# Performance work log

Hardware: AMD Instinct MI355X
Metric: run time of the kernel (lower is better)

The kernel has to match this reference:

```python
import jax, jax.numpy as jnp
import numpy as np

R = 1.1
SCALE = 100.0
BUMP_STEPS = 32
NUM_THETAS = 32
NUM_FEATURES = 128
N_NODES = 200000
NUM_GRAPHS = 128


def setup_inputs() -> dict:
    key = jax.random.key(0)
    k1, k2, k3 = jax.random.split(key, 3)
    x = jax.random.normal(k1, (N_NODES, NUM_FEATURES), dtype=jnp.float32)
    batch = jnp.sort(jax.random.randint(k2, (N_NODES,), 0, NUM_GRAPHS, dtype=jnp.int64))
    v = jax.random.uniform(k3, (NUM_THETAS, NUM_FEATURES), dtype=jnp.float32) - 0.5
    return {"x": x, "batch": batch, "num_graphs": NUM_GRAPHS, "v": v}


def reference(x, batch, num_graphs, v):
    # nh: node heights along each direction theta -> [N, T]
    nh = x @ v.T
    # linspace over filtration values -> [S]
    lin = jnp.linspace(-R, R, BUMP_STEPS, dtype=nh.dtype)
    # bump: sigmoid difference; second point is the constant pad value R
    # ecc: [N, S, T]  (node-major so segment_sum reduces the leading axis)
    ecc = (jax.nn.sigmoid(SCALE * (lin[None, :, None] - nh[:, None, :]))
           - jax.nn.sigmoid(SCALE * (lin - R))[None, :, None])
    # scatter-add per graph label -> [ng, S, T] == index_add over dim1 then movedim(0,1)
    ect = jax.ops.segment_sum(ecc, batch, num_segments=num_graphs)
    return ect
```

## Files before the change

kernel.cpp:

```cpp
#include <hip/hip_runtime.h>
#include <math.h>

#define N_NODES 200000
#define NF 128
#define NT 32
#define NS 32
#define NG 128
#define SPLITS 32
#define ATILE 64
#define ABLOCKS 3125
#define KSTRIDE 136
#define HPAD 33

typedef short bf16x8 __attribute__((ext_vector_type(8)));
typedef float floatx4 __attribute__((ext_vector_type(4)));

__device__ __forceinline__ float rcp_fast(float x) { return __builtin_amdgcn_rcpf(x); }

__device__ __forceinline__ void split_bf16(float f, unsigned short& h, unsigned short& l) {
    unsigned u  = __float_as_uint(f);
    unsigned r  = u + 0x7FFFu + ((u >> 16) & 1u);
    unsigned hb = r & 0xFFFF0000u;
    h = (unsigned short)(hb >> 16);
    float rem = f - __uint_as_float(hb);
    unsigned u2 = __float_as_uint(rem);
    unsigned r2 = u2 + 0x7FFFu + ((u2 >> 16) & 1u);
    l = (unsigned short)(r2 >> 16);
}

__global__ __launch_bounds__(256)
void offsets_kernel(const int* __restrict__ batch, int* __restrict__ off)
{
    int i = blockIdx.x * 256 + threadIdx.x;
    if (i >= N_NODES) return;
    int b  = batch[i];
    int bp = (i == 0) ? -1 : batch[i - 1];
    for (int g = bp + 1; g <= b; ++g) off[g] = i;
    if (i == N_NODES - 1)
        for (int g = b + 1; g <= NG; ++g) off[g] = N_NODES;
}

__global__ __launch_bounds__(256, 2)
void gemm_kernel(const float* __restrict__ x,
                 const float* __restrict__ v,
                 float* __restrict__ nh)
{
    __shared__ unsigned short xh[ATILE * KSTRIDE];
    __shared__ unsigned short xl[ATILE * KSTRIDE];
    __shared__ unsigned short vh[NT * KSTRIDE];
    __shared__ unsigned short vl[NT * KSTRIDE];

    const int tid = threadIdx.x;
    const int blk = blockIdx.x;

    #pragma unroll
    for (int j = 0; j < 8; ++j) {
        int idx4 = j * 256 + tid;
        int nn   = idx4 >> 5;
        int f4   = idx4 & 31;
        float4 val = *(const float4*)&x[(size_t)(blk * ATILE + nn) * NF + f4 * 4];
        unsigned short h0,h1,h2,h3,l0,l1,l2,l3;
        split_bf16(val.x, h0, l0); split_bf16(val.y, h1, l1);
        split_bf16(val.z, h2, l2); split_bf16(val.w, h3, l3);
        uint2 hh, ll;
        hh.x = (unsigned)h0 | ((unsigned)h1 << 16); hh.y = (unsigned)h2 | ((unsigned)h3 << 16);
        ll.x = (unsigned)l0 | ((unsigned)l1 << 16); ll.y = (unsigned)l2 | ((unsigned)l3 << 16);
        *(uint2*)&xh[nn * KSTRIDE + f4 * 4] = hh;
        *(uint2*)&xl[nn * KSTRIDE + f4 * 4] = ll;
    }
    #pragma unroll
    for (int j = 0; j < 4; ++j) {
        int idx4 = j * 256 + tid;
        int row  = idx4 >> 5;
        int f4   = idx4 & 31;
        float4 val = *(const float4*)&v[(size_t)row * NF + f4 * 4];
        unsigned short h0,h1,h2,h3,l0,l1,l2,l3;
        split_bf16(val.x, h0, l0); split_bf16(val.y, h1, l1);
        split_bf16(val.z, h2, l2); split_bf16(val.w, h3, l3);
        uint2 hh, ll;
        hh.x = (unsigned)h0 | ((unsigned)h1 << 16); hh.y = (unsigned)h2 | ((unsigned)h3 << 16);
        ll.x = (unsigned)l0 | ((unsigned)l1 << 16); ll.y = (unsigned)l2 | ((unsigned)l3 << 16);
        *(uint2*)&vh[row * KSTRIDE + f4 * 4] = hh;
        *(uint2*)&vl[row * KSTRIDE + f4 * 4] = ll;
    }
    __syncthreads();

    const int w    = tid >> 6;
    const int lane = tid & 63;
    const int mrow = lane & 15;
    const int quad = lane >> 4;

    const int abase  = (w * 16 + mrow) * KSTRIDE + quad * 8;
    const int b0base = mrow * KSTRIDE + quad * 8;
    const int b1base = (16 + mrow) * KSTRIDE + quad * 8;

    floatx4 acc0 = {0.f, 0.f, 0.f, 0.f};
    floatx4 acc1 = {0.f, 0.f, 0.f, 0.f};

    #pragma unroll
    for (int slice = 0; slice < 4; ++slice) {
        bf16x8 ah  = *(bf16x8*)&xh[abase  + slice * 32];
        bf16x8 al  = *(bf16x8*)&xl[abase  + slice * 32];
        bf16x8 bh0 = *(bf16x8*)&vh[b0base + slice * 32];
        bf16x8 bl0 = *(bf16x8*)&vl[b0base + slice * 32];
        bf16x8 bh1 = *(bf16x8*)&vh[b1base + slice * 32];
        bf16x8 bl1 = *(bf16x8*)&vl[b1base + slice * 32];
        acc0 = __builtin_amdgcn_mfma_f32_16x16x32_bf16(ah, bh0, acc0, 0, 0, 0);
        acc0 = __builtin_amdgcn_mfma_f32_16x16x32_bf16(ah, bl0, acc0, 0, 0, 0);
        acc0 = __builtin_amdgcn_mfma_f32_16x16x32_bf16(al, bh0, acc0, 0, 0, 0);
        acc1 = __builtin_amdgcn_mfma_f32_16x16x32_bf16(ah, bh1, acc1, 0, 0, 0);
        acc1 = __builtin_amdgcn_mfma_f32_16x16x32_bf16(ah, bl1, acc1, 0, 0, 0);
        acc1 = __builtin_amdgcn_mfma_f32_16x16x32_bf16(al, bh1, acc1, 0, 0, 0);
    }

    #pragma unroll
    for (int reg = 0; reg < 4; ++reg) {
        size_t node = (size_t)blk * ATILE + w * 16 + quad * 4 + reg;
        nh[node * NT + mrow]      = acc0[reg];
        nh[node * NT + 16 + mrow] = acc1[reg];
    }
}

__global__ __launch_bounds__(256, 8)
void sweep_kernel(const float* __restrict__ nh,
                  const int* __restrict__ off,
                  float* __restrict__ out)
{
    __shared__ unsigned hist[NT * HPAD];
    __shared__ float    corr[NT * HPAD];

    const int tid   = threadIdx.x;
    const int g     = blockIdx.x >> 5;
    const int split = blockIdx.x & (SPLITS - 1);

    for (int i = tid; i < NT * HPAD; i += 256) { hist[i] = 0u; corr[i] = 0.0f; }
    __syncthreads();

    const int g_start = off[g];
    const int g_end   = off[g + 1];
    const int count   = g_end - g_start;
    const int chunk   = (count + SPLITS - 1) / SPLITS;
    int my_start = g_start + split * chunk;
    if (my_start > g_end) my_start = g_end;
    int my_end = my_start + chunk;
    if (my_end > g_end) my_end = g_end;
    const int my_count = my_end - my_start;

    const float inv_dlin = 14.090909090909092f;
    const float Lw       = 10.23848093f;
    const float dlin     = 2.2f / 31.0f;
    const float L        = 144.26950408889634f;

    const int t = tid & 31;
    const int r = tid >> 5;

    for (int j = my_start + r; j < my_end; j += 8) {
        float h = nh[(size_t)j * NT + t];
        float z = fmaf(h, inv_dlin, 15.5f);
        int s_up = (int)ceilf(z);
        s_up = min(max(s_up, 0), 32);
        atomicAdd(&hist[t * HPAD + s_up], 1u);
        int s0 = (int)ceilf(z - 1.45f);
        #pragma unroll
        for (int i2 = 0; i2 < 3; ++i2) {
            int s = s0 + i2;
            float e   = __builtin_amdgcn_exp2f(Lw * (z - (float)s));
            float sig = rcp_fast(1.0f + e);
            float stp = (s >= s_up) ? 1.0f : 0.0f;
            float c   = sig - stp;
            if (s >= 0 && s <= 31) atomicAdd(&corr[t * HPAD + s], c);
        }
    }
    __syncthreads();

    {
        const int grp = tid >> 5;
        const int s   = tid & 31;
        for (int row = grp; row < NT; row += 8) {
            float val = (float)hist[row * HPAD + s];
            #pragma unroll
            for (int d = 1; d < 32; d <<= 1) {
                float nbr = __shfl_up(val, d, 32);
                if (s >= d) val += nbr;
            }
            corr[row * HPAD + s] += val;
        }
    }
    __syncthreads();

    const int sb = tid >> 5;
    #pragma unroll
    for (int k = 0; k < 4; ++k) {
        int s = sb + 8 * k;
        float lin_s = -1.1f + (float)s * dlin;
        float cs  = rcp_fast(1.0f + __builtin_amdgcn_exp2f(L * (1.1f - lin_s)));
        float val = corr[t * HPAD + s] - (float)my_count * cs;
        atomicAdd(&out[(size_t)g * (NS * NT) + s * NT + t], val);
    }
}

extern "C" void kernel_launch(void* const* d_in, const int* in_sizes, int n_in,
                              void* d_out, int out_size, void* d_ws, size_t ws_size,
                              hipStream_t stream) {
    const float* x     = (const float*)d_in[0];
    const int*   batch = (const int*)d_in[1];
    const float* v     = (const float*)d_in[3];
    float*       out   = (float*)d_out;

    int*   offs = (int*)d_ws;
    float* nh   = (float*)((char*)d_ws + 1024);

    hipMemsetAsync(d_out, 0, (size_t)out_size * sizeof(float), stream);
    offsets_kernel<<<dim3((N_NODES + 255) / 256), dim3(256), 0, stream>>>(batch, offs);
    gemm_kernel<<<dim3(ABLOCKS), dim3(256), 0, stream>>>(x, v, nh);
    sweep_kernel<<<dim3(NG * SPLITS), dim3(256), 0, stream>>>(nh, offs, out);
}
```

Before: 198.5 us.

## Fuse offsets, GEMM and histogram sweep into a single per-tile kernel

Replaces the offsets, GEMM and sweep kernels with one kernel. Each 64-node tile computes node heights in MFMA accumulators and immediately builds per-graph histograms and corrections in LDS, then atomically adds them to the output. This removes the global round trip of the node-height array, the offsets pass and two launches, and loads x straight into registers instead of staging it in LDS. The cost is extra per-tile work: a histogram clear, prefix scan and 1024 global atomics for every graph a tile touches. Global atomic contention on the output stays roughly the same as before.

```diff
diff --git a/kernel.cpp b/kernel.cpp
--- a/kernel.cpp
+++ b/kernel.cpp
@@ -6,10 +6,9 @@
 #define NT 32
 #define NS 32
 #define NG 128
-#define SPLITS 32
 #define ATILE 64
 #define ABLOCKS 3125
-#define KSTRIDE 136
+#define VSTRIDE 136
 #define HPAD 33
 
 typedef short bf16x8 __attribute__((ext_vector_type(8)));
@@ -28,46 +27,38 @@
     l = (unsigned short)(r2 >> 16);
 }
 
-__global__ __launch_bounds__(256)
-void offsets_kernel(const int* __restrict__ batch, int* __restrict__ off)
-{
-    int i = blockIdx.x * 256 + threadIdx.x;
-    if (i >= N_NODES) return;
-    int b  = batch[i];
-    int bp = (i == 0) ? -1 : batch[i - 1];
-    for (int g = bp + 1; g <= b; ++g) off[g] = i;
-    if (i == N_NODES - 1)
-        for (int g = b + 1; g <= NG; ++g) off[g] = N_NODES;
+__device__ __forceinline__ void split8(float4 a, float4 b, bf16x8& h8, bf16x8& l8) {
+    unsigned short h[8], l[8];
+    split_bf16(a.x, h[0], l[0]); split_bf16(a.y, h[1], l[1]);
+    split_bf16(a.z, h[2], l[2]); split_bf16(a.w, h[3], l[3]);
+    split_bf16(b.x, h[4], l[4]); split_bf16(b.y, h[5], l[5]);
+    split_bf16(b.z, h[6], l[6]); split_bf16(b.w, h[7], l[7]);
+    h8 = (bf16x8){(short)h[0],(short)h[1],(short)h[2],(short)h[3],
+                  (short)h[4],(short)h[5],(short)h[6],(short)h[7]};
+    l8 = (bf16x8){(short)l[0],(short)l[1],(short)l[2],(short)l[3],
+                  (short)l[4],(short)l[5],(short)l[6],(short)l[7]};
 }
 
-__global__ __launch_bounds__(256, 2)
-void gemm_kernel(const float* __restrict__ x,
-                 const float* __restrict__ v,
-                 float* __restrict__ nh)
+__global__ __launch_bounds__(256, 4)
+void ect_fused(const float* __restrict__ x,
+               const int* __restrict__ batch,
+               const float* __restrict__ v,
+               float* __restrict__ out)
 {
-    __shared__ unsigned short xh[ATILE * KSTRIDE];
-    __shared__ unsigned short xl[ATILE * KSTRIDE];
-    __shared__ unsigned short vh[NT * KSTRIDE];
-    __shared__ unsigned short vl[NT * KSTRIDE];
+    __shared__ unsigned short vh[NT * VSTRIDE];
+    __shared__ unsigned short vl[NT * VSTRIDE];
+    __shared__ int      batch_lds[ATILE];
+    __shared__ unsigned hist[NT * HPAD];
+    __shared__ float    corr[NT * HPAD];
+    __shared__ float    cnt_lds;
 
-    const int tid = threadIdx.x;
-    const int blk = blockIdx.x;
+    const int tid  = threadIdx.x;
+    const int blk  = blockIdx.x;
+    const int w    = tid >> 6;
+    const int lane = tid & 63;
+    const int mrow = lane & 15;
+    const int quad = lane >> 4;
 
-    #pragma unroll
-    for (int j = 0; j < 8; ++j) {
-        int idx4 = j * 256 + tid;
-        int nn   = idx4 >> 5;
-        int f4   = idx4 & 31;
-        float4 val = *(const float4*)&x[(size_t)(blk * ATILE + nn) * NF + f4 * 4];
-        unsigned short h0,h1,h2,h3,l0,l1,l2,l3;
-        split_bf16(val.x, h0, l0); split_bf16(val.y, h1, l1);
-        split_bf16(val.z, h2, l2); split_bf16(val.w, h3, l3);
-        uint2 hh, ll;
-        hh.x = (unsigned)h0 | ((unsigned)h1 << 16); hh.y = (unsigned)h2 | ((unsigned)h3 << 16);
-        ll.x = (unsigned)l0 | ((unsigned)l1 << 16); ll.y = (unsigned)l2 | ((unsigned)l3 << 16);
-        *(uint2*)&xh[nn * KSTRIDE + f4 * 4] = hh;
-        *(uint2*)&xl[nn * KSTRIDE + f4 * 4] = ll;
-    }
     #pragma unroll
     for (int j = 0; j < 4; ++j) {
         int idx4 = j * 256 + tid;
@@ -80,122 +71,111 @@
         uint2 hh, ll;
         hh.x = (unsigned)h0 | ((unsigned)h1 << 16); hh.y = (unsigned)h2 | ((unsigned)h3 << 16);
         ll.x = (unsigned)l0 | ((unsigned)l1 << 16); ll.y = (unsigned)l2 | ((unsigned)l3 << 16);
-        *(uint2*)&vh[row * KSTRIDE + f4 * 4] = hh;
-        *(uint2*)&vl[row * KSTRIDE + f4 * 4] = ll;
+        *(uint2*)&vh[row * VSTRIDE + f4 * 4] = hh;
+        *(uint2*)&vl[row * VSTRIDE + f4 * 4] = ll;
     }
-    __syncthreads();
+    if (tid < ATILE) batch_lds[tid] = batch[blk * ATILE + tid];
 
-    const int w    = tid >> 6;
-    const int lane = tid & 63;
-    const int mrow = lane & 15;
-    const int quad = lane >> 4;
-
-    const int abase  = (w * 16 + mrow) * KSTRIDE + quad * 8;
-    const int b0base = mrow * KSTRIDE + quad * 8;
-    const int b1base = (16 + mrow) * KSTRIDE + quad * 8;
+    const size_t arow = (size_t)blk * ATILE + w * 16 + mrow;
+    const float* __restrict__ xrow = x + arow * NF + quad * 8;
 
     floatx4 acc0 = {0.f, 0.f, 0.f, 0.f};
     floatx4 acc1 = {0.f, 0.f, 0.f, 0.f};
 
+    bf16x8 ah[4], al[4];
     #pragma unroll
     for (int slice = 0; slice < 4; ++slice) {
-        bf16x8 ah  = *(bf16x8*)&xh[abase  + slice * 32];
-        bf16x8 al  = *(bf16x8*)&xl[abase  + slice * 32];
+        float4 a0 = *(const float4*)&xrow[slice * 32];
+        float4 a1 = *(const float4*)&xrow[slice * 32 + 4];
+        split8(a0, a1, ah[slice], al[slice]);
+    }
+    __syncthreads();
+
+    const int b0base = mrow * VSTRIDE + quad * 8;
+    const int b1base = (16 + mrow) * VSTRIDE + quad * 8;
+    #pragma unroll
+    for (int slice = 0; slice < 4; ++slice) {
         bf16x8 bh0 = *(bf16x8*)&vh[b0base + slice * 32];
         bf16x8 bl0 = *(bf16x8*)&vl[b0base + slice * 32];
         bf16x8 bh1 = *(bf16x8*)&vh[b1base + slice * 32];
         bf16x8 bl1 = *(bf16x8*)&vl[b1base + slice * 32];
-        acc0 = __builtin_amdgcn_mfma_f32_16x16x32_bf16(ah, bh0, acc0, 0, 0, 0);
-        acc0 = __builtin_amdgcn_mfma_f32_16x16x32_bf16(ah, bl0, acc0, 0, 0, 0);
-        acc0 = __builtin_amdgcn_mfma_f32_16x16x32_bf16(al, bh0, acc0, 0, 0, 0);
-        acc1 = __builtin_amdgcn_mfma_f32_16x16x32_bf16(ah, bh1, acc1, 0, 0, 0);
-        acc1 = __builtin_amdgcn_mfma_f32_16x16x32_bf16(ah, bl1, acc1, 0, 0, 0);
-        acc1 = __builtin_amdgcn_mfma_f32_16x16x32_bf16(al, bh1, acc1, 0, 0, 0);
+        acc0 = __builtin_amdgcn_mfma_f32_16x16x32_bf16(ah[slice], bh0, acc0, 0, 0, 0);
+        acc0 = __builtin_amdgcn_mfma_f32_16x16x32_bf16(ah[slice], bl0, acc0, 0, 0, 0);
+        acc0 = __builtin_amdgcn_mfma_f32_16x16x32_bf16(al[slice], bh0, acc0, 0, 0, 0);
+        acc1 = __builtin_amdgcn_mfma_f32_16x16x32_bf16(ah[slice], bh1, acc1, 0, 0, 0);
+        acc1 = __builtin_amdgcn_mfma_f32_16x16x32_bf16(ah[slice], bl1, acc1, 0, 0, 0);
+        acc1 = __builtin_amdgcn_mfma_f32_16x16x32_bf16(al[slice], bh1, acc1, 0, 0, 0);
     }
-
-    #pragma unroll
-    for (int reg = 0; reg < 4; ++reg) {
-        size_t node = (size_t)blk * ATILE + w * 16 + quad * 4 + reg;
-        nh[node * NT + mrow]      = acc0[reg];
-        nh[node * NT + 16 + mrow] = acc1[reg];
-    }
-}
-
-__global__ __launch_bounds__(256, 8)
-void sweep_kernel(const float* __restrict__ nh,
-                  const int* __restrict__ off,
-                  float* __restrict__ out)
-{
-    __shared__ unsigned hist[NT * HPAD];
-    __shared__ float    corr[NT * HPAD];
-
-    const int tid   = threadIdx.x;
-    const int g     = blockIdx.x >> 5;
-    const int split = blockIdx.x & (SPLITS - 1);
-
-    for (int i = tid; i < NT * HPAD; i += 256) { hist[i] = 0u; corr[i] = 0.0f; }
-    __syncthreads();
-
-    const int g_start = off[g];
-    const int g_end   = off[g + 1];
-    const int count   = g_end - g_start;
-    const int chunk   = (count + SPLITS - 1) / SPLITS;
-    int my_start = g_start + split * chunk;
-    if (my_start > g_end) my_start = g_end;
-    int my_end = my_start + chunk;
-    if (my_end > g_end) my_end = g_end;
-    const int my_count = my_end - my_start;
 
     const float inv_dlin = 14.090909090909092f;
     const float Lw       = 10.23848093f;
     const float dlin     = 2.2f / 31.0f;
     const float L        = 144.26950408889634f;
 
-    const int t = tid & 31;
-    const int r = tid >> 5;
+    const int g_first = batch_lds[0];
+    const int g_last  = batch_lds[ATILE - 1];
 
-    for (int j = my_start + r; j < my_end; j += 8) {
-        float h = nh[(size_t)j * NT + t];
-        float z = fmaf(h, inv_dlin, 15.5f);
-        int s_up = (int)ceilf(z);
-        s_up = min(max(s_up, 0), 32);
-        atomicAdd(&hist[t * HPAD + s_up], 1u);
-        int s0 = (int)ceilf(z - 1.45f);
+    const int ft = tid & 31;
+    const int sb = tid >> 5;
+
+    for (int gp = g_first; gp <= g_last; ++gp) {
+        for (int i = tid; i < NT * HPAD; i += 256) { hist[i] = 0u; corr[i] = 0.0f; }
+        __syncthreads();
+
         #pragma unroll
-        for (int i2 = 0; i2 < 3; ++i2) {
-            int s = s0 + i2;
-            float e   = __builtin_amdgcn_exp2f(Lw * (z - (float)s));
-            float sig = rcp_fast(1.0f + e);
-            float stp = (s >= s_up) ? 1.0f : 0.0f;
-            float c   = sig - stp;
-            if (s >= 0 && s <= 31) atomicAdd(&corr[t * HPAD + s], c);
+        for (int reg = 0; reg < 4; ++reg) {
+            int n = w * 16 + quad * 4 + reg;
+            if (batch_lds[n] == gp) {
+                #pragma unroll
+                for (int half = 0; half < 2; ++half) {
+                    int   t = half ? (16 + mrow) : mrow;
+                    float h = half ? acc1[reg] : acc0[reg];
+                    float z = fmaf(h, inv_dlin, 15.5f);
+                    int s_up = (int)ceilf(z);
+                    s_up = min(max(s_up, 0), 32);
+                    atomicAdd(&hist[t * HPAD + s_up], 1u);
+                    int s0 = (int)ceilf(z - 1.45f);
+                    #pragma unroll
+                    for (int i2 = 0; i2 < 3; ++i2) {
+                        int s = s0 + i2;
+                        float e   = __builtin_amdgcn_exp2f(Lw * (z - (float)s));
+                        float sig = rcp_fast(1.0f + e);
+                        float stp = (s >= s_up) ? 1.0f : 0.0f;
+                        if (s >= 0 && s <= 31) atomicAdd(&corr[t * HPAD + s], sig - stp);
+                    }
+                }
+            }
         }
-    }
-    __syncthreads();
+        __syncthreads();
 
-    {
-        const int grp = tid >> 5;
-        const int s   = tid & 31;
-        for (int row = grp; row < NT; row += 8) {
-            float val = (float)hist[row * HPAD + s];
-            #pragma unroll
-            for (int d = 1; d < 32; d <<= 1) {
-                float nbr = __shfl_up(val, d, 32);
-                if (s >= d) val += nbr;
+        if (tid < ATILE) {
+            unsigned long long m = __ballot(batch_lds[tid] == gp);
+            if (tid == 0) cnt_lds = (float)__popcll(m);
+        }
+        {
+            const int grp = tid >> 5;
+            const int s   = tid & 31;
+            for (int row = grp; row < NT; row += 8) {
+                float val = (float)hist[row * HPAD + s];
+                #pragma unroll
+                for (int d = 1; d < 32; d <<= 1) {
+                    float nbr = __shfl_up(val, d, 32);
+                    if (s >= d) val += nbr;
+                }
+                corr[row * HPAD + s] += val;
             }
-            corr[row * HPAD + s] += val;
         }
-    }
-    __syncthreads();
+        __syncthreads();
 
-    const int sb = tid >> 5;
-    #pragma unroll
-    for (int k = 0; k < 4; ++k) {
-        int s = sb + 8 * k;
-        float lin_s = -1.1f + (float)s * dlin;
-        float cs  = rcp_fast(1.0f + __builtin_amdgcn_exp2f(L * (1.1f - lin_s)));
-        float val = corr[t * HPAD + s] - (float)my_count * cs;
-        atomicAdd(&out[(size_t)g * (NS * NT) + s * NT + t], val);
+        #pragma unroll
+        for (int k = 0; k < 4; ++k) {
+            int s = sb + 8 * k;
+            float lin_s = -1.1f + (float)s * dlin;
+            float cs  = rcp_fast(1.0f + __builtin_amdgcn_exp2f(L * (1.1f - lin_s)));
+            float val = corr[ft * HPAD + s] - cnt_lds * cs;
+            atomicAdd(&out[(size_t)gp * (NS * NT) + s * NT + ft], val);
+        }
+        if (gp < g_last) __syncthreads();
     }
 }
 
@@ -207,11 +187,6 @@
     const float* v     = (const float*)d_in[3];
     float*       out   = (float*)d_out;
 
-    int*   offs = (int*)d_ws;
-    float* nh   = (float*)((char*)d_ws + 1024);
-
     hipMemsetAsync(d_out, 0, (size_t)out_size * sizeof(float), stream);
-    offsets_kernel<<<dim3((N_NODES + 255) / 256), dim3(256), 0, stream>>>(batch, offs);
-    gemm_kernel<<<dim3(ABLOCKS), dim3(256), 0, stream>>>(x, v, nh);
-    sweep_kernel<<<dim3(NG * SPLITS), dim3(256), 0, stream>>>(nh, offs, out);
+    ect_fused<<<dim3(ABLOCKS), dim3(256), 0, stream>>>(x, batch, v, out);
 }
```

Result: faster. 168.8 us (-15.0%).
